# Performance work log

Hardware: AMD Instinct MI355X
Metric: run time of the kernel (lower is better)

Reference implementation:

```python
import jax, jax.numpy as jnp
import numpy as np


def _lstm_cell(x, h, c, Wih, Whh, b):
    # PyTorch LSTMCell gate order: i, f, g, o; b = b_ih + b_hh
    z = x @ Wih.T + h @ Whh.T + b
    i, f, g, o = jnp.split(z, 4, axis=-1)
    c_new = jax.nn.sigmoid(f) * c + jax.nn.sigmoid(i) * jnp.tanh(g)
    h_new = jax.nn.sigmoid(o) * jnp.tanh(c_new)
    return h_new, c_new


B, T, F, H, HOR, OUT = 16384, 96, 16, 64, 24, 16


def setup_inputs() -> dict:
    key = jax.random.key(0)
    ks = jax.random.split(key, 20)
    s = 1.0 / np.sqrt(H)

    def u(k, shape):
        return jax.random.uniform(k, shape, jnp.float32, -s, s)

    return {
        "X": jax.random.normal(ks[0], (B, T, F), jnp.float32),
        "bias": jax.random.normal(ks[1], (B, 1, OUT), jnp.float32),
        "X_mask": jnp.ones((B, T), dtype=bool),
        # encoder layer 0 (in=F) and layer 1 (in=H)
        "enc_Wih0": u(ks[2], (4 * H, F)), "enc_Whh0": u(ks[3], (4 * H, H)), "enc_b0": u(ks[4], (4 * H,)),
        "enc_Wih1": u(ks[5], (4 * H, H)), "enc_Whh1": u(ks[6], (4 * H, H)), "enc_b1": u(ks[7], (4 * H,)),
        # decoder layers (in=H)
        "dec_Wih0": u(ks[8], (4 * H, H)), "dec_Whh0": u(ks[9], (4 * H, H)), "dec_b0": u(ks[10], (4 * H,)),
        "dec_Wih1": u(ks[11], (4 * H, H)), "dec_Whh1": u(ks[12], (4 * H, H)), "dec_b1": u(ks[13], (4 * H,)),
        "reg_W1": u(ks[14], (H, H)), "reg_b1": u(ks[15], (H,)),
        "reg_W2": u(ks[16], (OUT, H)), "reg_b2": u(ks[17], (OUT,)),
    }


def reference(X, bias, X_mask,
              enc_Wih0, enc_Whh0, enc_b0, enc_Wih1, enc_Whh1, enc_b1,
              dec_Wih0, dec_Whh0, dec_b0, dec_Wih1, dec_Whh1, dec_b1,
              reg_W1, reg_b1, reg_W2, reg_b2):
    b = X.shape[0]
    z = jnp.zeros((b, H), X.dtype)

    # ---- encoder: scan over time, 2 stacked LSTMCells ----
    def enc_step(carry, x_t):
        h0, c0, h1, c1 = carry
        h0, c0 = _lstm_cell(x_t, h0, c0, enc_Wih0, enc_Whh0, enc_b0)
        h1, c1 = _lstm_cell(h0, h1, c1, enc_Wih1, enc_Whh1, enc_b1)
        return (h0, c0, h1, c1), None

    (h0, _, h1, _), _ = jax.lax.scan(enc_step, (z, z, z, z),
                                     jnp.swapaxes(X, 0, 1))  # [T,B,F]

    # ---- decoder: fresh c (zeros), h from encoder, h_t starts at top-layer h ----
    last_bias = bias[:, -1]  # [B, OUT]

    def dec_step(carry, _):
        h_t, dh0, dc0, dh1, dc1 = carry
        h_t, dc0 = _lstm_cell(h_t, dh0, dc0, dec_Wih0, dec_Whh0, dec_b0)
        dh0 = h_t
        h_t, dc1 = _lstm_cell(h_t, dh1, dc1, dec_Wih1, dec_Whh1, dec_b1)
        dh1 = h_t
        y = jax.nn.relu(h_t @ reg_W1.T + reg_b1) @ reg_W2.T + reg_b2
        y = y + last_bias  # add_last_step_val=True
        return (h_t, dh0, dc0, dh1, dc1), y

    _, ys = jax.lax.scan(dec_step, (h1, h0, z, h1, z), None, length=HOR)
    return jnp.swapaxes(ys, 0, 1)  # [B, horizon, OUT]
```

## Files before the change

### kernel.cpp

```cpp
#include <hip/hip_runtime.h>

typedef short v8s __attribute__((ext_vector_type(8)));
typedef float v4f __attribute__((ext_vector_type(4)));

__device__ __forceinline__ unsigned short f2bf(float f) {
    unsigned u = __builtin_bit_cast(unsigned, f);
    u += 0x7fffu + ((u >> 16) & 1u);
    return (unsigned short)(u >> 16);
}
__device__ __forceinline__ unsigned pk2(float a, float b) {
    return (unsigned)f2bf(a) | ((unsigned)f2bf(b) << 16);
}
__device__ __forceinline__ v8s pack8(float4 f0, float4 f1) {
    union { unsigned u[4]; v8s v; } r;
    r.u[0] = pk2(f0.x, f0.y); r.u[1] = pk2(f0.z, f0.w);
    r.u[2] = pk2(f1.x, f1.y); r.u[3] = pk2(f1.z, f1.w);
    return r.v;
}
__device__ __forceinline__ float sigm(float x) {
    float e = __builtin_amdgcn_exp2f(-1.44269504f * x);
    return __builtin_amdgcn_rcpf(1.0f + e);
}
__device__ __forceinline__ float tanh_(float x) {
    float e = __builtin_amdgcn_exp2f(2.88539008f * x);
    return 1.0f - 2.0f * __builtin_amdgcn_rcpf(1.0f + e);
}
__device__ __forceinline__ v4f mfma(v8s a, v8s b, v4f c) {
    return __builtin_amdgcn_mfma_f32_16x16x32_bf16(a, b, c, 0, 0, 0);
}
__device__ __forceinline__ v8s ldwf(const float* W, int rowElems, int n, int k0) {
    const float* p = W + (size_t)n * rowElems + k0;
    v8s r;
    #pragma unroll
    for (int j = 0; j < 8; ++j) r[j] = (short)f2bf(p[j]);
    return r;
}

__global__ __launch_bounds__(256, 2) void seq2seq(
    const float* __restrict__ X,
    const float* __restrict__ bias,
    const float* __restrict__ eWih0, const float* __restrict__ eWhh0, const float* __restrict__ eb0,
    const float* __restrict__ eWih1, const float* __restrict__ eWhh1, const float* __restrict__ eb1,
    const float* __restrict__ dWih0, const float* __restrict__ dWhh0, const float* __restrict__ db0,
    const float* __restrict__ dWih1, const float* __restrict__ dWhh1, const float* __restrict__ db1,
    const float* __restrict__ rW1, const float* __restrict__ rb1,
    const float* __restrict__ rW2, const float* __restrict__ rb2,
    float* __restrict__ out)
{
    __shared__ __align__(16) short sh0[2][2048];
    __shared__ __align__(16) short sh1[2][2048];
    __shared__ __align__(16) short sy1[2048];

    const int tid  = threadIdx.x;
    const int lane = tid & 63;
    const int w    = tid >> 6;
    const int lo   = lane & 15, hi = lane >> 4;
    const int wg   = blockIdx.x;

    for (int i = tid; i < 1024; i += 256) {
        ((int*)sh0)[1024 + i] = 0;
        ((int*)sh1)[1024 + i] = 0;
    }

    const int wsidx = (w >> 1) * 512 + (((2 * w) + (lo >> 3)) & 3) * 128 + hi * 32 + (lo & 7);

    v8s wf[4][4][2];
    float bz0[4], bz1[4];
    #pragma unroll
    for (int g = 0; g < 4; ++g) {
        const int n = (w + 4 * g) * 16 + lo;
        v8s z = {0, 0, 0, 0, 0, 0, 0, 0};
        wf[0][g][0] = (hi < 2) ? ldwf(eWih0, 16, n, (hi & 1) * 8) : z;
        wf[0][g][1] = z;
        #pragma unroll
        for (int kk = 0; kk < 2; ++kk) {
            wf[1][g][kk] = ldwf(eWhh0, 64, n, kk * 32 + hi * 8);
            wf[2][g][kk] = ldwf(eWih1, 64, n, kk * 32 + hi * 8);
            wf[3][g][kk] = ldwf(eWhh1, 64, n, kk * 32 + hi * 8);
        }
        bz0[g] = eb0[g * 64 + w * 16 + lo];
        bz1[g] = eb1[g * 64 + w * 16 + lo];
    }

    float c0[2][4] = {{0.f,0.f,0.f,0.f},{0.f,0.f,0.f,0.f}};
    float c1[2][4] = {{0.f,0.f,0.f,0.f},{0.f,0.f,0.f,0.f}};
    __syncthreads();

    const float* xb = X + (size_t)(wg * 32 + lo) * 1536 + (hi & 1) * 8;

    for (int t = 0; t < 96; ++t) {
        const int pw = t & 1, pr = pw ^ 1;
        v4f acc[4][2];
        #pragma unroll
        for (int g = 0; g < 4; ++g)
            #pragma unroll
            for (int mt = 0; mt < 2; ++mt)
                acc[g][mt] = (v4f){bz0[g], bz0[g], bz0[g], bz0[g]};
        #pragma unroll
        for (int mt = 0; mt < 2; ++mt) {
            const float* p = xb + (size_t)mt * 16 * 1536 + t * 16;
            const v8s ax = pack8(*(const float4*)p, *(const float4*)(p + 4));
            #pragma unroll
            for (int g = 0; g < 4; ++g) acc[g][mt] = mfma(ax, wf[0][g][0], acc[g][mt]);
        }
        #pragma unroll
        for (int kk = 0; kk < 2; ++kk)
            #pragma unroll
            for (int mt = 0; mt < 2; ++mt) {
                const v8s ah = *(const v8s*)&sh0[pr][(mt * 2 + kk) * 512 + lane * 8];
                #pragma unroll
                for (int g = 0; g < 4; ++g) acc[g][mt] = mfma(ah, wf[1][g][kk], acc[g][mt]);
            }
        #pragma unroll
        for (int mt = 0; mt < 2; ++mt) {
            float hh[4];
            #pragma unroll
            for (int q = 0; q < 4; ++q) {
                float cc = sigm(acc[1][mt][q]) * c0[mt][q] + sigm(acc[0][mt][q]) * tanh_(acc[2][mt][q]);
                c0[mt][q] = cc;
                hh[q] = sigm(acc[3][mt][q]) * tanh_(cc);
            }
            #pragma unroll
            for (int qp = 0; qp < 2; ++qp) {
                unsigned pk = pk2(hh[2 * qp], hh[2 * qp + 1]);
                short* b = &sh0[pw][wsidx + mt * 1024 + qp * 16];
                b[0] = (short)pk; b[8] = (short)(pk >> 16);
            }
        }
        __syncthreads();
        #pragma unroll
        for (int g = 0; g < 4; ++g)
            #pragma unroll
            for (int mt = 0; mt < 2; ++mt)
                acc[g][mt] = (v4f){bz1[g], bz1[g], bz1[g], bz1[g]};
        #pragma unroll
        for (int kk = 0; kk < 2; ++kk)
            #pragma unroll
            for (int mt = 0; mt < 2; ++mt) {
                const v8s ah = *(const v8s*)&sh0[pw][(mt * 2 + kk) * 512 + lane * 8];
                const v8s bh = *(const v8s*)&sh1[pr][(mt * 2 + kk) * 512 + lane * 8];
                #pragma unroll
                for (int g = 0; g < 4; ++g) {
                    acc[g][mt] = mfma(ah, wf[2][g][kk], acc[g][mt]);
                    acc[g][mt] = mfma(bh, wf[3][g][kk], acc[g][mt]);
                }
            }
        #pragma unroll
        for (int mt = 0; mt < 2; ++mt) {
            float hh[4];
            #pragma unroll
            for (int q = 0; q < 4; ++q) {
                float cc = sigm(acc[1][mt][q]) * c1[mt][q] + sigm(acc[0][mt][q]) * tanh_(acc[2][mt][q]);
                c1[mt][q] = cc;
                hh[q] = sigm(acc[3][mt][q]) * tanh_(cc);
            }
            #pragma unroll
            for (int qp = 0; qp < 2; ++qp) {
                unsigned pk = pk2(hh[2 * qp], hh[2 * qp + 1]);
                short* b = &sh1[pw][wsidx + mt * 1024 + qp * 16];
                b[0] = (short)pk; b[8] = (short)(pk >> 16);
            }
        }
    }
    __syncthreads();

    #pragma unroll
    for (int g = 0; g < 4; ++g) {
        const int n = (w + 4 * g) * 16 + lo;
        #pragma unroll
        for (int kk = 0; kk < 2; ++kk) {
            wf[0][g][kk] = ldwf(dWih0, 64, n, kk * 32 + hi * 8);
            wf[1][g][kk] = ldwf(dWhh0, 64, n, kk * 32 + hi * 8);
            wf[2][g][kk] = ldwf(dWih1, 64, n, kk * 32 + hi * 8);
            wf[3][g][kk] = ldwf(dWhh1, 64, n, kk * 32 + hi * 8);
        }
        bz0[g] = db0[g * 64 + w * 16 + lo];
        bz1[g] = db1[g * 64 + w * 16 + lo];
    }
    v8s w1f[2], w2f[2];
    #pragma unroll
    for (int kk = 0; kk < 2; ++kk) {
        w1f[kk] = ldwf(rW1, 64, w * 16 + lo, kk * 32 + hi * 8);
        w2f[kk] = ldwf(rW2, 64, lo, kk * 32 + hi * 8);
    }
    const float hb1 = rb1[w * 16 + lo];
    const float hb2 = rb2[lo];
    float lb[2][4];
    #pragma unroll
    for (int mt = 0; mt < 2; ++mt)
        #pragma unroll
        for (int q = 0; q < 4; ++q) {
            lb[mt][q] = bias[(size_t)(wg * 32 + mt * 16 + hi * 4 + q) * 16 + lo];
            c0[mt][q] = 0.f;
            c1[mt][q] = 0.f;
        }

    for (int s = 0; s < 24; ++s) {
        const int pw = s & 1, pr = pw ^ 1;
        v4f acc[4][2];
        #pragma unroll
        for (int g = 0; g < 4; ++g)
            #pragma unroll
            for (int mt = 0; mt < 2; ++mt)
                acc[g][mt] = (v4f){bz0[g], bz0[g], bz0[g], bz0[g]};
        #pragma unroll
        for (int kk = 0; kk < 2; ++kk)
            #pragma unroll
            for (int mt = 0; mt < 2; ++mt) {
                const v8s ah = *(const v8s*)&sh1[pr][(mt * 2 + kk) * 512 + lane * 8];
                const v8s bh = *(const v8s*)&sh0[pr][(mt * 2 + kk) * 512 + lane * 8];
                #pragma unroll
                for (int g = 0; g < 4; ++g) {
                    acc[g][mt] = mfma(ah, wf[0][g][kk], acc[g][mt]);
                    acc[g][mt] = mfma(bh, wf[1][g][kk], acc[g][mt]);
                }
            }
        #pragma unroll
        for (int mt = 0; mt < 2; ++mt) {
            float hh[4];
            #pragma unroll
            for (int q = 0; q < 4; ++q) {
                float cc = sigm(acc[1][mt][q]) * c0[mt][q] + sigm(acc[0][mt][q]) * tanh_(acc[2][mt][q]);
                c0[mt][q] = cc;
                hh[q] = sigm(acc[3][mt][q]) * tanh_(cc);
            }
            #pragma unroll
            for (int qp = 0; qp < 2; ++qp) {
                unsigned pk = pk2(hh[2 * qp], hh[2 * qp + 1]);
                short* b = &sh0[pw][wsidx + mt * 1024 + qp * 16];
                b[0] = (short)pk; b[8] = (short)(pk >> 16);
            }
        }
        __syncthreads();
        #pragma unroll
        for (int g = 0; g < 4; ++g)
            #pragma unroll
            for (int mt = 0; mt < 2; ++mt)
                acc[g][mt] = (v4f){bz1[g], bz1[g], bz1[g], bz1[g]};
        #pragma unroll
        for (int kk = 0; kk < 2; ++kk)
            #pragma unroll
            for (int mt = 0; mt < 2; ++mt) {
                const v8s ah = *(const v8s*)&sh0[pw][(mt * 2 + kk) * 512 + lane * 8];
                const v8s bh = *(const v8s*)&sh1[pr][(mt * 2 + kk) * 512 + lane * 8];
                #pragma unroll
                for (int g = 0; g < 4; ++g) {
                    acc[g][mt] = mfma(ah, wf[2][g][kk], acc[g][mt]);
                    acc[g][mt] = mfma(bh, wf[3][g][kk], acc[g][mt]);
                }
            }
        #pragma unroll
        for (int mt = 0; mt < 2; ++mt) {
            float hh[4];
            #pragma unroll
            for (int q = 0; q < 4; ++q) {
                float cc = sigm(acc[1][mt][q]) * c1[mt][q] + sigm(acc[0][mt][q]) * tanh_(acc[2][mt][q]);
                c1[mt][q] = cc;
                hh[q] = sigm(acc[3][mt][q]) * tanh_(cc);
            }
            #pragma unroll
            for (int qp = 0; qp < 2; ++qp) {
                unsigned pk = pk2(hh[2 * qp], hh[2 * qp + 1]);
                short* b = &sh1[pw][wsidx + mt * 1024 + qp * 16];
                b[0] = (short)pk; b[8] = (short)(pk >> 16);
            }
        }
        __syncthreads();
        v4f ay[2];
        #pragma unroll
        for (int mt = 0; mt < 2; ++mt) ay[mt] = (v4f){hb1, hb1, hb1, hb1};
        #pragma unroll
        for (int kk = 0; kk < 2; ++kk)
            #pragma unroll
            for (int mt = 0; mt < 2; ++mt) {
                const v8s ah = *(const v8s*)&sh1[pw][(mt * 2 + kk) * 512 + lane * 8];
                ay[mt] = mfma(ah, w1f[kk], ay[mt]);
            }
        #pragma unroll
        for (int mt = 0; mt < 2; ++mt) {
            #pragma unroll
            for (int qp = 0; qp < 2; ++qp) {
                unsigned pk = pk2(fmaxf(ay[mt][2 * qp], 0.f), fmaxf(ay[mt][2 * qp + 1], 0.f));
                short* b = &sy1[wsidx + mt * 1024 + qp * 16];
                b[0] = (short)pk; b[8] = (short)(pk >> 16);
            }
        }
        __syncthreads();
        if (w == 0) {
            v4f a2[2];
            #pragma unroll
            for (int mt = 0; mt < 2; ++mt) a2[mt] = (v4f){hb2, hb2, hb2, hb2};
            #pragma unroll
            for (int kk = 0; kk < 2; ++kk)
                #pragma unroll
                for (int mt = 0; mt < 2; ++mt) {
                    const v8s a = *(const v8s*)&sy1[(mt * 2 + kk) * 512 + lane * 8];
                    a2[mt] = mfma(a, w2f[kk], a2[mt]);
                }
            #pragma unroll
            for (int mt = 0; mt < 2; ++mt)
                #pragma unroll
                for (int q = 0; q < 4; ++q) {
                    size_t row = (size_t)(wg * 32 + mt * 16 + hi * 4 + q);
                    out[row * 384 + s * 16 + lo] = a2[mt][q] + lb[mt][q];
                }
        }
    }
}

extern "C" void kernel_launch(void* const* d_in, const int* in_sizes, int n_in,
                              void* d_out, int out_size, void* d_ws, size_t ws_size,
                              hipStream_t stream) {
    seq2seq<<<dim3(512), dim3(256), 0, stream>>>(
        (const float*)d_in[0],
        (const float*)d_in[1],
        (const float*)d_in[3],  (const float*)d_in[4],  (const float*)d_in[5],
        (const float*)d_in[6],  (const float*)d_in[7],  (const float*)d_in[8],
        (const float*)d_in[9],  (const float*)d_in[10], (const float*)d_in[11],
        (const float*)d_in[12], (const float*)d_in[13], (const float*)d_in[14],
        (const float*)d_in[15], (const float*)d_in[16],
        (const float*)d_in[17], (const float*)d_in[18],
        (float*)d_out);
}
```

Before: 615.9 us.

## Halve batch rows per block, double grid, raise occupancy, use hardware bf16 pack

Each workgroup now handles 16 batch rows instead of 32, so the grid doubles to 1024 blocks. Per-thread accumulators and shared buffers shrink, and launch bounds move to 4 blocks per CU. The goal is more waves in flight to hide the serial recurrence latency of MFMA, transcendental and barrier work, since 512 blocks underfill the 256 CUs. Software bf16 rounding is replaced by the v_cvt_pk_bf16_f32 instruction. The trade-off is less MFMA work per barrier and weight fragments reloaded by twice as many blocks.

```diff
diff --git a/kernel.cpp b/kernel.cpp
--- a/kernel.cpp
+++ b/kernel.cpp
@@ -3,18 +3,15 @@
 typedef short v8s __attribute__((ext_vector_type(8)));
 typedef float v4f __attribute__((ext_vector_type(4)));
 
-__device__ __forceinline__ unsigned short f2bf(float f) {
-    unsigned u = __builtin_bit_cast(unsigned, f);
-    u += 0x7fffu + ((u >> 16) & 1u);
-    return (unsigned short)(u >> 16);
-}
-__device__ __forceinline__ unsigned pk2(float a, float b) {
-    return (unsigned)f2bf(a) | ((unsigned)f2bf(b) << 16);
+__device__ __forceinline__ unsigned cvtpk(float lo, float hi) {
+    unsigned r;
+    asm("v_cvt_pk_bf16_f32 %0, %1, %2" : "=v"(r) : "v"(lo), "v"(hi));
+    return r;
 }
 __device__ __forceinline__ v8s pack8(float4 f0, float4 f1) {
     union { unsigned u[4]; v8s v; } r;
-    r.u[0] = pk2(f0.x, f0.y); r.u[1] = pk2(f0.z, f0.w);
-    r.u[2] = pk2(f1.x, f1.y); r.u[3] = pk2(f1.z, f1.w);
+    r.u[0] = cvtpk(f0.x, f0.y); r.u[1] = cvtpk(f0.z, f0.w);
+    r.u[2] = cvtpk(f1.x, f1.y); r.u[3] = cvtpk(f1.z, f1.w);
     return r.v;
 }
 __device__ __forceinline__ float sigm(float x) {
@@ -30,13 +27,13 @@
 }
 __device__ __forceinline__ v8s ldwf(const float* W, int rowElems, int n, int k0) {
     const float* p = W + (size_t)n * rowElems + k0;
-    v8s r;
-    #pragma unroll
-    for (int j = 0; j < 8; ++j) r[j] = (short)f2bf(p[j]);
-    return r;
-}
-
-__global__ __launch_bounds__(256, 2) void seq2seq(
+    union { unsigned u[4]; v8s v; } r;
+    #pragma unroll
+    for (int j = 0; j < 4; ++j) r.u[j] = cvtpk(p[2 * j], p[2 * j + 1]);
+    return r.v;
+}
+
+__global__ __launch_bounds__(256, 4) void seq2seq(
     const float* __restrict__ X,
     const float* __restrict__ bias,
     const float* __restrict__ eWih0, const float* __restrict__ eWhh0, const float* __restrict__ eb0,
@@ -47,9 +44,9 @@
     const float* __restrict__ rW2, const float* __restrict__ rb2,
     float* __restrict__ out)
 {
-    __shared__ __align__(16) short sh0[2][2048];
-    __shared__ __align__(16) short sh1[2][2048];
-    __shared__ __align__(16) short sy1[2048];
+    __shared__ __align__(16) short sh0[2][1024];
+    __shared__ __align__(16) short sh1[2][1024];
+    __shared__ __align__(16) short sy1[1024];
 
     const int tid  = threadIdx.x;
     const int lane = tid & 63;
@@ -57,9 +54,9 @@
     const int lo   = lane & 15, hi = lane >> 4;
     const int wg   = blockIdx.x;
 
-    for (int i = tid; i < 1024; i += 256) {
-        ((int*)sh0)[1024 + i] = 0;
-        ((int*)sh1)[1024 + i] = 0;
+    for (int i = tid; i < 512; i += 256) {
+        ((int*)sh0)[512 + i] = 0;
+        ((int*)sh1)[512 + i] = 0;
     }
 
     const int wsidx = (w >> 1) * 512 + (((2 * w) + (lo >> 3)) & 3) * 128 + hi * 32 + (lo & 7);
@@ -82,82 +79,71 @@
         bz1[g] = eb1[g * 64 + w * 16 + lo];
     }
 
-    float c0[2][4] = {{0.f,0.f,0.f,0.f},{0.f,0.f,0.f,0.f}};
-    float c1[2][4] = {{0.f,0.f,0.f,0.f},{0.f,0.f,0.f,0.f}};
+    float c0[4] = {0.f, 0.f, 0.f, 0.f};
+    float c1[4] = {0.f, 0.f, 0.f, 0.f};
     __syncthreads();
 
-    const float* xb = X + (size_t)(wg * 32 + lo) * 1536 + (hi & 1) * 8;
+    const float* xb = X + (size_t)(wg * 16 + lo) * 1536 + (hi & 1) * 8;
 
     for (int t = 0; t < 96; ++t) {
         const int pw = t & 1, pr = pw ^ 1;
-        v4f acc[4][2];
-        #pragma unroll
-        for (int g = 0; g < 4; ++g)
-            #pragma unroll
-            for (int mt = 0; mt < 2; ++mt)
-                acc[g][mt] = (v4f){bz0[g], bz0[g], bz0[g], bz0[g]};
-        #pragma unroll
-        for (int mt = 0; mt < 2; ++mt) {
-            const float* p = xb + (size_t)mt * 16 * 1536 + t * 16;
+        v4f acc[4];
+        #pragma unroll
+        for (int g = 0; g < 4; ++g)
+            acc[g] = (v4f){bz0[g], bz0[g], bz0[g], bz0[g]};
+        #pragma unroll
+        for (int kk = 0; kk < 2; ++kk) {
+            const v8s ah = *(const v8s*)&sh0[pr][kk * 512 + lane * 8];
+            #pragma unroll
+            for (int g = 0; g < 4; ++g) acc[g] = mfma(ah, wf[1][g][kk], acc[g]);
+        }
+        {
+            const float* p = xb + t * 16;
             const v8s ax = pack8(*(const float4*)p, *(const float4*)(p + 4));
             #pragma unroll
-            for (int g = 0; g < 4; ++g) acc[g][mt] = mfma(ax, wf[0][g][0], acc[g][mt]);
-        }
-        #pragma unroll
-        for (int kk = 0; kk < 2; ++kk)
-            #pragma unroll
-            for (int mt = 0; mt < 2; ++mt) {
-                const v8s ah = *(const v8s*)&sh0[pr][(mt * 2 + kk) * 512 + lane * 8];
-                #pragma unroll
-                for (int g = 0; g < 4; ++g) acc[g][mt] = mfma(ah, wf[1][g][kk], acc[g][mt]);
-            }
-        #pragma unroll
-        for (int mt = 0; mt < 2; ++mt) {
-            float hh[4];
-            #pragma unroll
-            for (int q = 0; q < 4; ++q) {
-                float cc = sigm(acc[1][mt][q]) * c0[mt][q] + sigm(acc[0][mt][q]) * tanh_(acc[2][mt][q]);
-                c0[mt][q] = cc;
-                hh[q] = sigm(acc[3][mt][q]) * tanh_(cc);
-            }
-            #pragma unroll
-            for (int qp = 0; qp < 2; ++qp) {
-                unsigned pk = pk2(hh[2 * qp], hh[2 * qp + 1]);
-                short* b = &sh0[pw][wsidx + mt * 1024 + qp * 16];
-                b[0] = (short)pk; b[8] = (short)(pk >> 16);
-            }
-        }
-        __syncthreads();
-        #pragma unroll
-        for (int g = 0; g < 4; ++g)
-            #pragma unroll
-            for (int mt = 0; mt < 2; ++mt)
-                acc[g][mt] = (v4f){bz1[g], bz1[g], bz1[g], bz1[g]};
-        #pragma unroll
-        for (int kk = 0; kk < 2; ++kk)
-            #pragma unroll
-            for (int mt = 0; mt < 2; ++mt) {
-                const v8s ah = *(const v8s*)&sh0[pw][(mt * 2 + kk) * 512 + lane * 8];
-                const v8s bh = *(const v8s*)&sh1[pr][(mt * 2 + kk) * 512 + lane * 8];
-                #pragma unroll
-                for (int g = 0; g < 4; ++g) {
-                    acc[g][mt] = mfma(ah, wf[2][g][kk], acc[g][mt]);
-                    acc[g][mt] = mfma(bh, wf[3][g][kk], acc[g][mt]);
-                }
-            }
-        #pragma unroll
-        for (int mt = 0; mt < 2; ++mt) {
-            float hh[4];
-            #pragma unroll
-            for (int q = 0; q < 4; ++q) {
-                float cc = sigm(acc[1][mt][q]) * c1[mt][q] + sigm(acc[0][mt][q]) * tanh_(acc[2][mt][q]);
-                c1[mt][q] = cc;
-                hh[q] = sigm(acc[3][mt][q]) * tanh_(cc);
-            }
-            #pragma unroll
-            for (int qp = 0; qp < 2; ++qp) {
-                unsigned pk = pk2(hh[2 * qp], hh[2 * qp + 1]);
-                short* b = &sh1[pw][wsidx + mt * 1024 + qp * 16];
+            for (int g = 0; g < 4; ++g) acc[g] = mfma(ax, wf[0][g][0], acc[g]);
+        }
+        {
+            float hh[4];
+            #pragma unroll
+            for (int q = 0; q < 4; ++q) {
+                float cc = sigm(acc[1][q]) * c0[q] + sigm(acc[0][q]) * tanh_(acc[2][q]);
+                c0[q] = cc;
+                hh[q] = sigm(acc[3][q]) * tanh_(cc);
+            }
+            #pragma unroll
+            for (int qp = 0; qp < 2; ++qp) {
+                unsigned pk = cvtpk(hh[2 * qp], hh[2 * qp + 1]);
+                short* b = &sh0[pw][wsidx + qp * 16];
+                b[0] = (short)pk; b[8] = (short)(pk >> 16);
+            }
+        }
+        __syncthreads();
+        #pragma unroll
+        for (int g = 0; g < 4; ++g)
+            acc[g] = (v4f){bz1[g], bz1[g], bz1[g], bz1[g]};
+        #pragma unroll
+        for (int kk = 0; kk < 2; ++kk) {
+            const v8s ah = *(const v8s*)&sh0[pw][kk * 512 + lane * 8];
+            const v8s bh = *(const v8s*)&sh1[pr][kk * 512 + lane * 8];
+            #pragma unroll
+            for (int g = 0; g < 4; ++g) {
+                acc[g] = mfma(ah, wf[2][g][kk], acc[g]);
+                acc[g] = mfma(bh, wf[3][g][kk], acc[g]);
+            }
+        }
+        {
+            float hh[4];
+            #pragma unroll
+            for (int q = 0; q < 4; ++q) {
+                float cc = sigm(acc[1][q]) * c1[q] + sigm(acc[0][q]) * tanh_(acc[2][q]);
+                c1[q] = cc;
+                hh[q] = sigm(acc[3][q]) * tanh_(cc);
+            }
+            #pragma unroll
+            for (int qp = 0; qp < 2; ++qp) {
+                unsigned pk = cvtpk(hh[2 * qp], hh[2 * qp + 1]);
+                short* b = &sh1[pw][wsidx + qp * 16];
                 b[0] = (short)pk; b[8] = (short)(pk >> 16);
             }
         }
@@ -185,125 +171,100 @@
     }
     const float hb1 = rb1[w * 16 + lo];
     const float hb2 = rb2[lo];
-    float lb[2][4];
-    #pragma unroll
-    for (int mt = 0; mt < 2; ++mt)
-        #pragma unroll
-        for (int q = 0; q < 4; ++q) {
-            lb[mt][q] = bias[(size_t)(wg * 32 + mt * 16 + hi * 4 + q) * 16 + lo];
-            c0[mt][q] = 0.f;
-            c1[mt][q] = 0.f;
-        }
+    float lb[4];
+    #pragma unroll
+    for (int q = 0; q < 4; ++q) {
+        lb[q] = bias[(size_t)(wg * 16 + hi * 4 + q) * 16 + lo];
+        c0[q] = 0.f;
+        c1[q] = 0.f;
+    }
 
     for (int s = 0; s < 24; ++s) {
         const int pw = s & 1, pr = pw ^ 1;
-        v4f acc[4][2];
-        #pragma unroll
-        for (int g = 0; g < 4; ++g)
-            #pragma unroll
-            for (int mt = 0; mt < 2; ++mt)
-                acc[g][mt] = (v4f){bz0[g], bz0[g], bz0[g], bz0[g]};
-        #pragma unroll
-        for (int kk = 0; kk < 2; ++kk)
-            #pragma unroll
-            for (int mt = 0; mt < 2; ++mt) {
-                const v8s ah = *(const v8s*)&sh1[pr][(mt * 2 + kk) * 512 + lane * 8];
-                const v8s bh = *(const v8s*)&sh0[pr][(mt * 2 + kk) * 512 + lane * 8];
-                #pragma unroll
-                for (int g = 0; g < 4; ++g) {
-                    acc[g][mt] = mfma(ah, wf[0][g][kk], acc[g][mt]);
-                    acc[g][mt] = mfma(bh, wf[1][g][kk], acc[g][mt]);
-                }
-            }
-        #pragma unroll
-        for (int mt = 0; mt < 2; ++mt) {
-            float hh[4];
-            #pragma unroll
-            for (int q = 0; q < 4; ++q) {
-                float cc = sigm(acc[1][mt][q]) * c0[mt][q] + sigm(acc[0][mt][q]) * tanh_(acc[2][mt][q]);
-                c0[mt][q] = cc;
-                hh[q] = sigm(acc[3][mt][q]) * tanh_(cc);
-            }
-            #pragma unroll
-            for (int qp = 0; qp < 2; ++qp) {
-                unsigned pk = pk2(hh[2 * qp], hh[2 * qp + 1]);
-                short* b = &sh0[pw][wsidx + mt * 1024 + qp * 16];
-                b[0] = (short)pk; b[8] = (short)(pk >> 16);
-            }
-        }
-        __syncthreads();
-        #pragma unroll
-        for (int g = 0; g < 4; ++g)
-            #pragma unroll
-            for (int mt = 0; mt < 2; ++mt)
-                acc[g][mt] = (v4f){bz1[g], bz1[g], bz1[g], bz1[g]};
-        #pragma unroll
-        for (int kk = 0; kk < 2; ++kk)
-            #pragma unroll
-            for (int mt = 0; mt < 2; ++mt) {
-                const v8s ah = *(const v8s*)&sh0[pw][(mt * 2 + kk) * 512 + lane * 8];
-                const v8s bh = *(const v8s*)&sh1[pr][(mt * 2 + kk) * 512 + lane * 8];
-                #pragma unroll
-                for (int g = 0; g < 4; ++g) {
-                    acc[g][mt] = mfma(ah, wf[2][g][kk], acc[g][mt]);
-                    acc[g][mt] = mfma(bh, wf[3][g][kk], acc[g][mt]);
-                }
-            }
-        #pragma unroll
-        for (int mt = 0; mt < 2; ++mt) {
-            float hh[4];
-            #pragma unroll
-            for (int q = 0; q < 4; ++q) {
-                float cc = sigm(acc[1][mt][q]) * c1[mt][q] + sigm(acc[0][mt][q]) * tanh_(acc[2][mt][q]);
-                c1[mt][q] = cc;
-                hh[q] = sigm(acc[3][mt][q]) * tanh_(cc);
-            }
-            #pragma unroll
-            for (int qp = 0; qp < 2; ++qp) {
-                unsigned pk = pk2(hh[2 * qp], hh[2 * qp + 1]);
-                short* b = &sh1[pw][wsidx + mt * 1024 + qp * 16];
-                b[0] = (short)pk; b[8] = (short)(pk >> 16);
-            }
-        }
-        __syncthreads();
-        v4f ay[2];
-        #pragma unroll
-        for (int mt = 0; mt < 2; ++mt) ay[mt] = (v4f){hb1, hb1, hb1, hb1};
-        #pragma unroll
-        for (int kk = 0; kk < 2; ++kk)
-            #pragma unroll
-            for (int mt = 0; mt < 2; ++mt) {
-                const v8s ah = *(const v8s*)&sh1[pw][(mt * 2 + kk) * 512 + lane * 8];
-                ay[mt] = mfma(ah, w1f[kk], ay[mt]);
-            }
-        #pragma unroll
-        for (int mt = 0; mt < 2; ++mt) {
-            #pragma unroll
-            for (int qp = 0; qp < 2; ++qp) {
-                unsigned pk = pk2(fmaxf(ay[mt][2 * qp], 0.f), fmaxf(ay[mt][2 * qp + 1], 0.f));
-                short* b = &sy1[wsidx + mt * 1024 + qp * 16];
-                b[0] = (short)pk; b[8] = (short)(pk >> 16);
-            }
+        v4f acc[4];
+        #pragma unroll
+        for (int g = 0; g < 4; ++g)
+            acc[g] = (v4f){bz0[g], bz0[g], bz0[g], bz0[g]};
+        #pragma unroll
+        for (int kk = 0; kk < 2; ++kk) {
+            const v8s ah = *(const v8s*)&sh1[pr][kk * 512 + lane * 8];
+            const v8s bh = *(const v8s*)&sh0[pr][kk * 512 + lane * 8];
+            #pragma unroll
+            for (int g = 0; g < 4; ++g) {
+                acc[g] = mfma(ah, wf[0][g][kk], acc[g]);
+                acc[g] = mfma(bh, wf[1][g][kk], acc[g]);
+            }
+        }
+        {
+            float hh[4];
+            #pragma unroll
+            for (int q = 0; q < 4; ++q) {
+                float cc = sigm(acc[1][q]) * c0[q] + sigm(acc[0][q]) * tanh_(acc[2][q]);
+                c0[q] = cc;
+                hh[q] = sigm(acc[3][q]) * tanh_(cc);
+            }
+            #pragma unroll
+            for (int qp = 0; qp < 2; ++qp) {
+                unsigned pk = cvtpk(hh[2 * qp], hh[2 * qp + 1]);
+                short* b = &sh0[pw][wsidx + qp * 16];
+                b[0] = (short)pk; b[8] = (short)(pk >> 16);
+            }
+        }
+        __syncthreads();
+        #pragma unroll
+        for (int g = 0; g < 4; ++g)
+            acc[g] = (v4f){bz1[g], bz1[g], bz1[g], bz1[g]};
+        #pragma unroll
+        for (int kk = 0; kk < 2; ++kk) {
+            const v8s ah = *(const v8s*)&sh0[pw][kk * 512 + lane * 8];
+            const v8s bh = *(const v8s*)&sh1[pr][kk * 512 + lane * 8];
+            #pragma unroll
+            for (int g = 0; g < 4; ++g) {
+                acc[g] = mfma(ah, wf[2][g][kk], acc[g]);
+                acc[g] = mfma(bh, wf[3][g][kk], acc[g]);
+            }
+        }
+        {
+            float hh[4];
+            #pragma unroll
+            for (int q = 0; q < 4; ++q) {
+                float cc = sigm(acc[1][q]) * c1[q] + sigm(acc[0][q]) * tanh_(acc[2][q]);
+                c1[q] = cc;
+                hh[q] = sigm(acc[3][q]) * tanh_(cc);
+            }
+            #pragma unroll
+            for (int qp = 0; qp < 2; ++qp) {
+                unsigned pk = cvtpk(hh[2 * qp], hh[2 * qp + 1]);
+                short* b = &sh1[pw][wsidx + qp * 16];
+                b[0] = (short)pk; b[8] = (short)(pk >> 16);
+            }
+        }
+        __syncthreads();
+        v4f ay = (v4f){hb1, hb1, hb1, hb1};
+        #pragma unroll
+        for (int kk = 0; kk < 2; ++kk) {
+            const v8s ah = *(const v8s*)&sh1[pw][kk * 512 + lane * 8];
+            ay = mfma(ah, w1f[kk], ay);
+        }
+        #pragma unroll
+        for (int qp = 0; qp < 2; ++qp) {
+            unsigned pk = cvtpk(fmaxf(ay[2 * qp], 0.f), fmaxf(ay[2 * qp + 1], 0.f));
+            short* b = &sy1[wsidx + qp * 16];
+            b[0] = (short)pk; b[8] = (short)(pk >> 16);
         }
         __syncthreads();
         if (w == 0) {
-            v4f a2[2];
-            #pragma unroll
-            for (int mt = 0; mt < 2; ++mt) a2[mt] = (v4f){hb2, hb2, hb2, hb2};
-            #pragma unroll
-            for (int kk = 0; kk < 2; ++kk)
-                #pragma unroll
-                for (int mt = 0; mt < 2; ++mt) {
-                    const v8s a = *(const v8s*)&sy1[(mt * 2 + kk) * 512 + lane * 8];
-                    a2[mt] = mfma(a, w2f[kk], a2[mt]);
-                }
-            #pragma unroll
-            for (int mt = 0; mt < 2; ++mt)
-                #pragma unroll
-                for (int q = 0; q < 4; ++q) {
-                    size_t row = (size_t)(wg * 32 + mt * 16 + hi * 4 + q);
-                    out[row * 384 + s * 16 + lo] = a2[mt][q] + lb[mt][q];
-                }
+            v4f a2 = (v4f){hb2, hb2, hb2, hb2};
+            #pragma unroll
+            for (int kk = 0; kk < 2; ++kk) {
+                const v8s a = *(const v8s*)&sy1[kk * 512 + lane * 8];
+                a2 = mfma(a, w2f[kk], a2);
+            }
+            #pragma unroll
+            for (int q = 0; q < 4; ++q) {
+                size_t row = (size_t)(wg * 16 + hi * 4 + q);
+                out[row * 384 + s * 16 + lo] = a2[q] + lb[q];
+            }
         }
     }
 }
@@ -311,7 +272,7 @@
 extern "C" void kernel_launch(void* const* d_in, const int* in_sizes, int n_in,
                               void* d_out, int out_size, void* d_ws, size_t ws_size,
                               hipStream_t stream) {
-    seq2seq<<<dim3(512), dim3(256), 0, stream>>>(
+    seq2seq<<<dim3(1024), dim3(256), 0, stream>>>(
         (const float*)d_in[0],
         (const float*)d_in[1],
         (const float*)d_in[3],  (const float*)d_in[4],  (const float*)d_in[5],
```

After: 1.365 ms. 2.22x slower.

## Use hardware bf16 pack conversion and defer decoder output projection one step

Applied to the files above, without the earlier changes.

Replaces the software round-to-nearest bf16 conversion with the v_cvt_pk_bf16_f32 instruction everywhere, cutting ALU work on the recurrent critical path. Also moves the second regressor matmul and output store for step s-1 into step s, after the first barrier. This removes one __syncthreads per decoder step, and the final step's output is handled after the loop. The deferred projection relies on the existing barriers to keep sy1 reads ordered against the next write, and it adds a tail block after the loop.

```diff
diff --git a/kernel.cpp b/kernel.cpp
--- a/kernel.cpp
+++ b/kernel.cpp
@@ -3,18 +3,15 @@
 typedef short v8s __attribute__((ext_vector_type(8)));
 typedef float v4f __attribute__((ext_vector_type(4)));
 
-__device__ __forceinline__ unsigned short f2bf(float f) {
-    unsigned u = __builtin_bit_cast(unsigned, f);
-    u += 0x7fffu + ((u >> 16) & 1u);
-    return (unsigned short)(u >> 16);
-}
-__device__ __forceinline__ unsigned pk2(float a, float b) {
-    return (unsigned)f2bf(a) | ((unsigned)f2bf(b) << 16);
+__device__ __forceinline__ unsigned cvtpk(float lo, float hi) {
+    unsigned r;
+    asm("v_cvt_pk_bf16_f32 %0, %1, %2" : "=v"(r) : "v"(lo), "v"(hi));
+    return r;
 }
 __device__ __forceinline__ v8s pack8(float4 f0, float4 f1) {
     union { unsigned u[4]; v8s v; } r;
-    r.u[0] = pk2(f0.x, f0.y); r.u[1] = pk2(f0.z, f0.w);
-    r.u[2] = pk2(f1.x, f1.y); r.u[3] = pk2(f1.z, f1.w);
+    r.u[0] = cvtpk(f0.x, f0.y); r.u[1] = cvtpk(f0.z, f0.w);
+    r.u[2] = cvtpk(f1.x, f1.y); r.u[3] = cvtpk(f1.z, f1.w);
     return r.v;
 }
 __device__ __forceinline__ float sigm(float x) {
@@ -30,10 +27,10 @@
 }
 __device__ __forceinline__ v8s ldwf(const float* W, int rowElems, int n, int k0) {
     const float* p = W + (size_t)n * rowElems + k0;
-    v8s r;
-    #pragma unroll
-    for (int j = 0; j < 8; ++j) r[j] = (short)f2bf(p[j]);
-    return r;
+    union { unsigned u[4]; v8s v; } r;
+    #pragma unroll
+    for (int j = 0; j < 4; ++j) r.u[j] = cvtpk(p[2 * j], p[2 * j + 1]);
+    return r.v;
 }
 
 __global__ __launch_bounds__(256, 2) void seq2seq(
@@ -122,7 +119,7 @@
             }
             #pragma unroll
             for (int qp = 0; qp < 2; ++qp) {
-                unsigned pk = pk2(hh[2 * qp], hh[2 * qp + 1]);
+                unsigned pk = cvtpk(hh[2 * qp], hh[2 * qp + 1]);
                 short* b = &sh0[pw][wsidx + mt * 1024 + qp * 16];
                 b[0] = (short)pk; b[8] = (short)(pk >> 16);
             }
@@ -156,7 +153,7 @@
             }
             #pragma unroll
             for (int qp = 0; qp < 2; ++qp) {
-                unsigned pk = pk2(hh[2 * qp], hh[2 * qp + 1]);
+                unsigned pk = cvtpk(hh[2 * qp], hh[2 * qp + 1]);
                 short* b = &sh1[pw][wsidx + mt * 1024 + qp * 16];
                 b[0] = (short)pk; b[8] = (short)(pk >> 16);
             }
@@ -226,12 +223,31 @@
             }
             #pragma unroll
             for (int qp = 0; qp < 2; ++qp) {
-                unsigned pk = pk2(hh[2 * qp], hh[2 * qp + 1]);
+                unsigned pk = cvtpk(hh[2 * qp], hh[2 * qp + 1]);
                 short* b = &sh0[pw][wsidx + mt * 1024 + qp * 16];
                 b[0] = (short)pk; b[8] = (short)(pk >> 16);
             }
         }
         __syncthreads();
+        if (w == 0 && s > 0) {
+            v4f a2[2];
+            #pragma unroll
+            for (int mt = 0; mt < 2; ++mt) a2[mt] = (v4f){hb2, hb2, hb2, hb2};
+            #pragma unroll
+            for (int kk = 0; kk < 2; ++kk)
+                #pragma unroll
+                for (int mt = 0; mt < 2; ++mt) {
+                    const v8s a = *(const v8s*)&sy1[(mt * 2 + kk) * 512 + lane * 8];
+                    a2[mt] = mfma(a, w2f[kk], a2[mt]);
+                }
+            #pragma unroll
+            for (int mt = 0; mt < 2; ++mt)
+                #pragma unroll
+                for (int q = 0; q < 4; ++q) {
+                    size_t row = (size_t)(wg * 32 + mt * 16 + hi * 4 + q);
+                    out[row * 384 + (s - 1) * 16 + lo] = a2[mt][q] + lb[mt][q];
+                }
+        }
         #pragma unroll
         for (int g = 0; g < 4; ++g)
             #pragma unroll
@@ -260,7 +276,7 @@
             }
             #pragma unroll
             for (int qp = 0; qp < 2; ++qp) {
-                unsigned pk = pk2(hh[2 * qp], hh[2 * qp + 1]);
+                unsigned pk = cvtpk(hh[2 * qp], hh[2 * qp + 1]);
                 short* b = &sh1[pw][wsidx + mt * 1024 + qp * 16];
                 b[0] = (short)pk; b[8] = (short)(pk >> 16);
             }
@@ -280,31 +296,31 @@
         for (int mt = 0; mt < 2; ++mt) {
             #pragma unroll
             for (int qp = 0; qp < 2; ++qp) {
-                unsigned pk = pk2(fmaxf(ay[mt][2 * qp], 0.f), fmaxf(ay[mt][2 * qp + 1], 0.f));
+                unsigned pk = cvtpk(fmaxf(ay[mt][2 * qp], 0.f), fmaxf(ay[mt][2 * qp + 1], 0.f));
                 short* b = &sy1[wsidx + mt * 1024 + qp * 16];
                 b[0] = (short)pk; b[8] = (short)(pk >> 16);
             }
         }
-        __syncthreads();
-        if (w == 0) {
-            v4f a2[2];
-            #pragma unroll
-            for (int mt = 0; mt < 2; ++mt) a2[mt] = (v4f){hb2, hb2, hb2, hb2};
-            #pragma unroll
-            for (int kk = 0; kk < 2; ++kk)
-                #pragma unroll
-                for (int mt = 0; mt < 2; ++mt) {
-                    const v8s a = *(const v8s*)&sy1[(mt * 2 + kk) * 512 + lane * 8];
-                    a2[mt] = mfma(a, w2f[kk], a2[mt]);
-                }
-            #pragma unroll
-            for (int mt = 0; mt < 2; ++mt)
-                #pragma unroll
-                for (int q = 0; q < 4; ++q) {
-                    size_t row = (size_t)(wg * 32 + mt * 16 + hi * 4 + q);
-                    out[row * 384 + s * 16 + lo] = a2[mt][q] + lb[mt][q];
-                }
-        }
+    }
+    __syncthreads();
+    if (w == 0) {
+        v4f a2[2];
+        #pragma unroll
+        for (int mt = 0; mt < 2; ++mt) a2[mt] = (v4f){hb2, hb2, hb2, hb2};
+        #pragma unroll
+        for (int kk = 0; kk < 2; ++kk)
+            #pragma unroll
+            for (int mt = 0; mt < 2; ++mt) {
+                const v8s a = *(const v8s*)&sy1[(mt * 2 + kk) * 512 + lane * 8];
+                a2[mt] = mfma(a, w2f[kk], a2[mt]);
+            }
+        #pragma unroll
+        for (int mt = 0; mt < 2; ++mt)
+            #pragma unroll
+            for (int q = 0; q < 4; ++q) {
+                size_t row = (size_t)(wg * 32 + mt * 16 + hi * 4 + q);
+                out[row * 384 + 23 * 16 + lo] = a2[mt][q] + lb[mt][q];
+            }
     }
 }
 
```

New measurement: 590.5 us. 4.1% less time.
